# Kernel optimization log

Measured on AMD Instinct MI355X. Metric: run time of the kernel, lower is better.

## Reference

```python
import jax, jax.numpy as jnp
import numpy as np

N, D = 8192, 128

def setup_inputs() -> dict:
    key = jax.random.key(0)
    kq, kk, kv = jax.random.split(key, 3)
    return {
        "query": jax.random.normal(kq, (N, D), dtype=jnp.float32),
        "key": jax.random.normal(kk, (N, D), dtype=jnp.float32),
        "value": jax.random.normal(kv, (N, D), dtype=jnp.float32),
    }

def reference(query, key, value):
    # FlashAttentionV1 computes exact (non-causal, unmasked) softmax attention:
    # softmax(Q K^T / sqrt(d)) V, via tiled online softmax. The math is
    # identical to the dense formulation below.
    d = query.shape[-1]
    scores = jnp.einsum('qd,kd->qk', query, key) / jnp.sqrt(jnp.asarray(d, query.dtype))
    probs = jax.nn.softmax(scores, axis=-1)
    return jnp.einsum('qk,kd->qd', probs, value)
```

## Files before the change

### kernel.cpp

```cpp
#include <hip/hip_runtime.h>

#define NTOK 8192
#define DH   128
#define QBLK 128
#define KVB  64

typedef __attribute__((ext_vector_type(8)))  short bf16x8;
typedef __attribute__((ext_vector_type(16))) float f32x16;
typedef __attribute__((ext_vector_type(4)))  unsigned short u16x4;

typedef __attribute__((address_space(1))) const void gv_t;
typedef __attribute__((address_space(3))) void sv_t;

static __device__ __forceinline__ unsigned short f2bf(float x) {
  union { float f; unsigned int u; } a; a.f = x;
  unsigned int r = a.u + 0x7FFFu + ((a.u >> 16) & 1u);
  return (unsigned short)(r >> 16);
}

static __device__ __forceinline__ unsigned pk2(float lo, float hi) {
  unsigned r;
  asm("v_cvt_pk_bf16_f32 %0, %1, %2" : "=v"(r) : "v"(lo), "v"(hi));
  return r;
}

static __device__ __forceinline__ f32x16 zero16() {
  f32x16 v;
  #pragma unroll
  for (int i = 0; i < 16; ++i) v[i] = 0.f;
  return v;
}

__global__ __launch_bounds__(256)
void fa_prep(const float* __restrict__ Kg, const float* __restrict__ Vg,
             char* __restrict__ Kimg, char* __restrict__ Vimg)
{
  const int t = blockIdx.x;
  const int tid = threadIdx.x;

  {
    const int krow = tid >> 2;
    const int kcg  = (tid & 3) * 32;
    const float* src = Kg + ((size_t)t * KVB + krow) * DH + kcg;
    char* drow = Kimg + (size_t)t * 16384 + krow * 256;
    const int sw = (krow & 15) << 4;
    #pragma unroll
    for (int w = 0; w < 4; ++w) {
      float4 a = *reinterpret_cast<const float4*>(src + w * 8);
      float4 b = *reinterpret_cast<const float4*>(src + w * 8 + 4);
      union { bf16x8 v; unsigned short u[8]; } f;
      f.u[0] = f2bf(a.x); f.u[1] = f2bf(a.y); f.u[2] = f2bf(a.z); f.u[3] = f2bf(a.w);
      f.u[4] = f2bf(b.x); f.u[5] = f2bf(b.y); f.u[6] = f2bf(b.z); f.u[7] = f2bf(b.w);
      *reinterpret_cast<bf16x8*>(drow + ((kcg * 2 + w * 16) ^ sw)) = f.v;
    }
  }

  {
    #pragma unroll
    for (int it = 0; it < 2; ++it) {
      int task = tid + it * 256;
      int kvl  = (task & 15) * 4;
      int d0   = (task >> 4) * 4;
      const float* src = Vg + ((size_t)t * KVB + kvl) * DH + d0;
      float4 r0 = *reinterpret_cast<const float4*>(src);
      float4 r1 = *reinterpret_cast<const float4*>(src + DH);
      float4 r2 = *reinterpret_cast<const float4*>(src + 2 * DH);
      float4 r3 = *reinterpret_cast<const float4*>(src + 3 * DH);
      char* base = Vimg + (size_t)t * 16384;
      const int bb = kvl * 2;
      { int d = d0 + 0;
        u16x4 w4 = (u16x4){f2bf(r0.x), f2bf(r1.x), f2bf(r2.x), f2bf(r3.x)};
        *reinterpret_cast<u16x4*>(base + d * 128 + (bb ^ ((d & 15) << 3))) = w4; }
      { int d = d0 + 1;
        u16x4 w4 = (u16x4){f2bf(r0.y), f2bf(r1.y), f2bf(r2.y), f2bf(r3.y)};
        *reinterpret_cast<u16x4*>(base + d * 128 + (bb ^ ((d & 15) << 3))) = w4; }
      { int d = d0 + 2;
        u16x4 w4 = (u16x4){f2bf(r0.z), f2bf(r1.z), f2bf(r2.z), f2bf(r3.z)};
        *reinterpret_cast<u16x4*>(base + d * 128 + (bb ^ ((d & 15) << 3))) = w4; }
      { int d = d0 + 3;
        u16x4 w4 = (u16x4){f2bf(r0.w), f2bf(r1.w), f2bf(r2.w), f2bf(r3.w)};
        *reinterpret_cast<u16x4*>(base + d * 128 + (bb ^ ((d & 15) << 3))) = w4; }
    }
  }
}

static __device__ __forceinline__ void softmax_half(
    const f32x16& st, float& m_run, float& l_run, f32x16* oacc,
    bf16x8& pfa, bf16x8& pfb)
{
  float pmax = st[0];
  #pragma unroll
  for (int r = 1; r < 16; ++r) pmax = fmaxf(pmax, st[r]);
  pmax = fmaxf(pmax, __shfl_xor(pmax, 32));
  if (!__all(pmax <= m_run + 8.f)) {
    const float m_new = fmaxf(m_run, pmax);
    const float corr  = (m_run > -1e30f) ? exp2f(m_run - m_new) : 0.f;
    l_run *= corr;
    #pragma unroll
    for (int i = 0; i < 4; ++i) oacc[i] = oacc[i] * corr;
    m_run = m_new;
  }
  float psum = 0.f;
  unsigned w[8];
  #pragma unroll
  for (int i = 0; i < 8; ++i) {
    const float e0 = exp2f(st[2 * i]     - m_run);
    const float e1 = exp2f(st[2 * i + 1] - m_run);
    psum += e0 + e1;
    w[i] = pk2(e0, e1);
  }
  psum += __shfl_xor(psum, 32);
  l_run += psum;
  union { bf16x8 v; unsigned u[4]; } fa, fb;
  fa.u[0] = w[0]; fa.u[1] = w[1]; fa.u[2] = w[2]; fa.u[3] = w[3];
  fb.u[0] = w[4]; fb.u[1] = w[5]; fb.u[2] = w[6]; fb.u[3] = w[7];
  pfa = fa.v; pfb = fb.v;
}

__global__ __launch_bounds__(256, 2)
void fa_fwd(const float* __restrict__ Qg, const char* __restrict__ Kimg,
            const char* __restrict__ Vimg, float* __restrict__ Od,
            float* __restrict__ Mp, float* __restrict__ Lp,
            int ksplit, int chunk_len)
{
  __shared__ __align__(16) char smem[2][32768];
  const int tid  = threadIdx.x;
  const int lane = tid & 63;
  const int wv   = tid >> 6;
  const int l31  = lane & 31;
  const int hi   = lane >> 5;

  const int q     = blockIdx.x * QBLK + wv * 32 + l31;
  const int chunk = blockIdx.y;
  const float QSCALE = 0.1275313310087464f;

  const int tile0 = (chunk * chunk_len) >> 6;
  const int nst   = chunk_len >> 6;

  bf16x8 qf[8];
  {
    const float* qs = Qg + (size_t)q * DH + hi * 8;
    #pragma unroll
    for (int kc = 0; kc < 8; ++kc) {
      float4 a = *reinterpret_cast<const float4*>(qs + kc * 16);
      float4 b = *reinterpret_cast<const float4*>(qs + kc * 16 + 4);
      union { bf16x8 v; unsigned u[4]; } f;
      f.u[0] = pk2(a.x * QSCALE, a.y * QSCALE);
      f.u[1] = pk2(a.z * QSCALE, a.w * QSCALE);
      f.u[2] = pk2(b.x * QSCALE, b.y * QSCALE);
      f.u[3] = pk2(b.z * QSCALE, b.w * QSCALE);
      qf[kc] = f.v;
    }
  }

  const char* gbase = (wv < 2 ? Kimg : Vimg);
  const size_t goff = (size_t)(wv & 1) * 8192 + (size_t)lane * 16;
  const int    loff = (wv < 2 ? 0 : 16384) + (wv & 1) * 8192;

#define STAGE(B, T) do {                                                      \
    const char* _s = gbase + (size_t)(T) * 16384 + goff;                      \
    char* _d = &smem[B][loff];                                                \
    _Pragma("unroll")                                                         \
    for (int _i = 0; _i < 8; ++_i)                                            \
      __builtin_amdgcn_global_load_lds((gv_t*)(_s + _i * 1024),               \
                                       (sv_t*)(_d + _i * 1024), 16, 0, 0);    \
  } while (0)

  STAGE(0, tile0);
  if (nst > 1) STAGE(1, tile0 + 1);

  f32x16 oacc[4];
  #pragma unroll
  for (int i = 0; i < 4; ++i) oacc[i] = zero16();
  float m_run = -INFINITY, l_run = 0.f;

  int cur = 0;
  for (int t = 0; t < nst; ++t) {
    if (t + 1 < nst) asm volatile("s_waitcnt vmcnt(8)" ::: "memory");
    else             asm volatile("s_waitcnt vmcnt(0)" ::: "memory");
    __builtin_amdgcn_sched_barrier(0);
    __builtin_amdgcn_s_barrier();

    const char* smK = smem[cur];
    const char* smV = smem[cur] + 16384;
    const int swk = (l31 & 15) << 4;
    const int swv = (l31 & 15) << 3;

    f32x16 st0 = zero16(), st1 = zero16();
    __builtin_amdgcn_s_setprio(1);
    #pragma unroll
    for (int kc = 0; kc < 8; ++kc) {
      const int cb = (kc * 32 + hi * 16) ^ swk;
      bf16x8 a0 = *reinterpret_cast<const bf16x8*>(smK + l31 * 256 + cb);
      st0 = __builtin_amdgcn_mfma_f32_32x32x16_bf16(a0, qf[kc], st0, 0, 0, 0);
      bf16x8 a1 = *reinterpret_cast<const bf16x8*>(smK + (l31 + 32) * 256 + cb);
      st1 = __builtin_amdgcn_mfma_f32_32x32x16_bf16(a1, qf[kc], st1, 0, 0, 0);
    }
    __builtin_amdgcn_s_setprio(0);

    bf16x8 pf0a, pf0b;
    softmax_half(st0, m_run, l_run, oacc, pf0a, pf0b);
    __builtin_amdgcn_s_setprio(1);
    #pragma unroll
    for (int c = 0; c < 2; ++c) {
      const bf16x8 pb = c ? pf0b : pf0a;
      #pragma unroll
      for (int dt = 0; dt < 4; ++dt) {
        const char* vb = smV + (dt * 32 + l31) * 128;
        union { bf16x8 v; u16x4 h[2]; } a;
        a.h[0] = *reinterpret_cast<const u16x4*>(vb + ((c * 32 + 8 * hi) ^ swv));
        a.h[1] = *reinterpret_cast<const u16x4*>(vb + ((c * 32 + 16 + 8 * hi) ^ swv));
        oacc[dt] = __builtin_amdgcn_mfma_f32_32x32x16_bf16(a.v, pb, oacc[dt], 0, 0, 0);
      }
    }
    __builtin_amdgcn_s_setprio(0);

    bf16x8 pf1a, pf1b;
    softmax_half(st1, m_run, l_run, oacc, pf1a, pf1b);
    __builtin_amdgcn_s_setprio(1);
    #pragma unroll
    for (int c = 2; c < 4; ++c) {
      const bf16x8 pb = (c & 1) ? pf1b : pf1a;
      #pragma unroll
      for (int dt = 0; dt < 4; ++dt) {
        const char* vb = smV + (dt * 32 + l31) * 128;
        union { bf16x8 v; u16x4 h[2]; } a;
        a.h[0] = *reinterpret_cast<const u16x4*>(vb + ((c * 32 + 8 * hi) ^ swv));
        a.h[1] = *reinterpret_cast<const u16x4*>(vb + ((c * 32 + 16 + 8 * hi) ^ swv));
        oacc[dt] = __builtin_amdgcn_mfma_f32_32x32x16_bf16(a.v, pb, oacc[dt], 0, 0, 0);
      }
    }
    __builtin_amdgcn_s_setprio(0);

    __builtin_amdgcn_s_barrier();
    if (t + 2 < nst) STAGE(cur, tile0 + t + 2);
    cur ^= 1;
  }
#undef STAGE

  char* base = &smem[0][0] + wv * 16384;
  const float scale = (ksplit == 1) ? (1.f / l_run) : 1.f;
  #pragma unroll
  for (int dt = 0; dt < 4; ++dt)
    #pragma unroll
    for (int rg = 0; rg < 4; ++rg)
      #pragma unroll
      for (int j = 0; j < 4; ++j) {
        const int d = dt * 32 + rg * 8 + hi * 4 + j;
        *reinterpret_cast<float*>(base + d * 128 + l31 * 4) =
            oacc[dt][rg * 4 + j] * scale;
      }
  const int qloc = lane >> 1;
  const int dh   = lane & 1;
  float* dst = ((ksplit == 1) ? Od : Od + (size_t)chunk * NTOK * DH)
               + (size_t)(blockIdx.x * QBLK + wv * 32 + qloc) * DH + dh * 64;
  #pragma unroll
  for (int i4 = 0; i4 < 16; ++i4) {
    float4 v;
    v.x = *reinterpret_cast<float*>(base + (dh * 64 + i4 * 4 + 0) * 128 + qloc * 4);
    v.y = *reinterpret_cast<float*>(base + (dh * 64 + i4 * 4 + 1) * 128 + qloc * 4);
    v.z = *reinterpret_cast<float*>(base + (dh * 64 + i4 * 4 + 2) * 128 + qloc * 4);
    v.w = *reinterpret_cast<float*>(base + (dh * 64 + i4 * 4 + 3) * 128 + qloc * 4);
    *reinterpret_cast<float4*>(dst + i4 * 4) = v;
  }
  if (ksplit > 1 && lane < 32) {
    const int qg = blockIdx.x * QBLK + wv * 32 + lane;
    Mp[chunk * NTOK + qg] = m_run;
    Lp[chunk * NTOK + qg] = l_run;
  }
}

__global__ __launch_bounds__(256)
void fa_combine(const float* __restrict__ Op, const float* __restrict__ Mp,
                const float* __restrict__ Lp, float* __restrict__ out, int ksplit)
{
  const int gid = blockIdx.x * 256 + threadIdx.x;
  const int q   = gid >> 5;
  const int dv  = (gid & 31) * 4;
  float mx = -INFINITY;
  for (int c = 0; c < ksplit; ++c) mx = fmaxf(mx, Mp[c * NTOK + q]);
  float den = 0.f;
  float ax = 0.f, ay = 0.f, az = 0.f, aw = 0.f;
  for (int c = 0; c < ksplit; ++c) {
    const float w = exp2f(Mp[c * NTOK + q] - mx);
    den += w * Lp[c * NTOK + q];
    float4 o = *reinterpret_cast<const float4*>(Op + (size_t)c * NTOK * DH + (size_t)q * DH + dv);
    ax += w * o.x; ay += w * o.y; az += w * o.z; aw += w * o.w;
  }
  const float r = 1.f / den;
  float4 res; res.x = ax * r; res.y = ay * r; res.z = az * r; res.w = aw * r;
  *reinterpret_cast<float4*>(out + (size_t)q * DH + dv) = res;
}

extern "C" void kernel_launch(void* const* d_in, const int* in_sizes, int n_in,
                              void* d_out, int out_size, void* d_ws, size_t ws_size,
                              hipStream_t stream)
{
  const float* Q = (const float*)d_in[0];
  const float* K = (const float*)d_in[1];
  const float* V = (const float*)d_in[2];
  float* out = (float*)d_out;

  auto need = [](size_t ks) {
    return ks * (size_t)NTOK * DH * 4 + 2 * ks * (size_t)NTOK * 4;
  };
  int KS = (ws_size >= need(8)) ? 8 : (ws_size >= need(4)) ? 4 : 2;

  char* Kimg = (char*)d_out;
  char* Vimg = Kimg + (size_t)NTOK * 256;

  float* Op = (float*)d_ws;
  float* Mp = Op + (size_t)KS * NTOK * DH;
  float* Lp = Mp + (size_t)KS * NTOK;

  fa_prep<<<NTOK / KVB, 256, 0, stream>>>(K, V, Kimg, Vimg);
  fa_fwd<<<dim3(NTOK / QBLK, KS), 256, 0, stream>>>(Q, Kimg, Vimg, Op, Mp, Lp,
                                                    KS, NTOK / KS);
  fa_combine<<<NTOK * DH / 4 / 256, 256, 0, stream>>>(Op, Mp, Lp, out, KS);
}
```

Measured before the change: 75.33 us.

## Double query block to 8 waves sharing KV tiles and raise K-split

Doubles the query block to 256 rows and the workgroup to 512 threads, so eight waves share each staged K/V tile and each wave issues half as many global-to-LDS loads. Removes the per-tile cross-half shuffles for the row sum, deferring that reduction to the epilogue; the max shuffle now runs only when a rescale is needed. The epilogue runs in two barrier-separated phases to reuse the LDS buffer, and the default KV split rises to 16. The tighter launch bounds (512 threads, 4 blocks) may force heavy register spilling given the accumulators held per wave.

```diff
diff --git a/kernel.cpp b/kernel.cpp
--- a/kernel.cpp
+++ b/kernel.cpp
@@ -2,7 +2,7 @@
 
 #define NTOK 8192
 #define DH   128
-#define QBLK 128
+#define QBLK 256
 #define KVB  64
 
 typedef __attribute__((ext_vector_type(8)))  short bf16x8;
@@ -91,8 +91,8 @@
   float pmax = st[0];
   #pragma unroll
   for (int r = 1; r < 16; ++r) pmax = fmaxf(pmax, st[r]);
-  pmax = fmaxf(pmax, __shfl_xor(pmax, 32));
   if (!__all(pmax <= m_run + 8.f)) {
+    pmax = fmaxf(pmax, __shfl_xor(pmax, 32));
     const float m_new = fmaxf(m_run, pmax);
     const float corr  = (m_run > -1e30f) ? exp2f(m_run - m_new) : 0.f;
     l_run *= corr;
@@ -109,7 +109,6 @@
     psum += e0 + e1;
     w[i] = pk2(e0, e1);
   }
-  psum += __shfl_xor(psum, 32);
   l_run += psum;
   union { bf16x8 v; unsigned u[4]; } fa, fb;
   fa.u[0] = w[0]; fa.u[1] = w[1]; fa.u[2] = w[2]; fa.u[3] = w[3];
@@ -117,7 +116,7 @@
   pfa = fa.v; pfb = fb.v;
 }
 
-__global__ __launch_bounds__(256, 2)
+__global__ __launch_bounds__(512, 4)
 void fa_fwd(const float* __restrict__ Qg, const char* __restrict__ Kimg,
             const char* __restrict__ Vimg, float* __restrict__ Od,
             float* __restrict__ Mp, float* __restrict__ Lp,
@@ -153,15 +152,15 @@
     }
   }
 
-  const char* gbase = (wv < 2 ? Kimg : Vimg);
-  const size_t goff = (size_t)(wv & 1) * 8192 + (size_t)lane * 16;
-  const int    loff = (wv < 2 ? 0 : 16384) + (wv & 1) * 8192;
+  const char* gbase = (wv < 4 ? Kimg : Vimg);
+  const size_t goff = (size_t)(wv & 3) * 4096 + (size_t)lane * 16;
+  const int    loff = (wv < 4 ? 0 : 16384) + (wv & 3) * 4096;
 
 #define STAGE(B, T) do {                                                      \
     const char* _s = gbase + (size_t)(T) * 16384 + goff;                      \
     char* _d = &smem[B][loff];                                                \
     _Pragma("unroll")                                                         \
-    for (int _i = 0; _i < 8; ++_i)                                            \
+    for (int _i = 0; _i < 4; ++_i)                                            \
       __builtin_amdgcn_global_load_lds((gv_t*)(_s + _i * 1024),               \
                                        (sv_t*)(_d + _i * 1024), 16, 0, 0);    \
   } while (0)
@@ -176,7 +175,7 @@
 
   int cur = 0;
   for (int t = 0; t < nst; ++t) {
-    if (t + 1 < nst) asm volatile("s_waitcnt vmcnt(8)" ::: "memory");
+    if (t + 1 < nst) asm volatile("s_waitcnt vmcnt(4)" ::: "memory");
     else             asm volatile("s_waitcnt vmcnt(0)" ::: "memory");
     __builtin_amdgcn_sched_barrier(0);
     __builtin_amdgcn_s_barrier();
@@ -238,35 +237,47 @@
   }
 #undef STAGE
 
-  char* base = &smem[0][0] + wv * 16384;
-  const float scale = (ksplit == 1) ? (1.f / l_run) : 1.f;
-  #pragma unroll
-  for (int dt = 0; dt < 4; ++dt)
-    #pragma unroll
-    for (int rg = 0; rg < 4; ++rg)
-      #pragma unroll
-      for (int j = 0; j < 4; ++j) {
-        const int d = dt * 32 + rg * 8 + hi * 4 + j;
-        *reinterpret_cast<float*>(base + d * 128 + l31 * 4) =
-            oacc[dt][rg * 4 + j] * scale;
-      }
-  const int qloc = lane >> 1;
-  const int dh   = lane & 1;
-  float* dst = ((ksplit == 1) ? Od : Od + (size_t)chunk * NTOK * DH)
-               + (size_t)(blockIdx.x * QBLK + wv * 32 + qloc) * DH + dh * 64;
-  #pragma unroll
-  for (int i4 = 0; i4 < 16; ++i4) {
-    float4 v;
-    v.x = *reinterpret_cast<float*>(base + (dh * 64 + i4 * 4 + 0) * 128 + qloc * 4);
-    v.y = *reinterpret_cast<float*>(base + (dh * 64 + i4 * 4 + 1) * 128 + qloc * 4);
-    v.z = *reinterpret_cast<float*>(base + (dh * 64 + i4 * 4 + 2) * 128 + qloc * 4);
-    v.w = *reinterpret_cast<float*>(base + (dh * 64 + i4 * 4 + 3) * 128 + qloc * 4);
-    *reinterpret_cast<float4*>(dst + i4 * 4) = v;
-  }
+  const float l_tot = l_run + __shfl_xor(l_run, 32);
+
+  char* base = &smem[0][0] + (wv & 3) * 16384;
+  const float scale = (ksplit == 1) ? (1.f / l_tot) : 1.f;
+  float* dstb = ((ksplit == 1) ? Od : Od + (size_t)chunk * NTOK * DH);
+
+#define EPILOGUE() do {                                                        \
+    _Pragma("unroll")                                                          \
+    for (int dt = 0; dt < 4; ++dt)                                             \
+      _Pragma("unroll")                                                        \
+      for (int rg = 0; rg < 4; ++rg)                                           \
+        _Pragma("unroll")                                                      \
+        for (int j = 0; j < 4; ++j) {                                          \
+          const int d = dt * 32 + rg * 8 + hi * 4 + j;                         \
+          *reinterpret_cast<float*>(base + d * 128 + l31 * 4) =                \
+              oacc[dt][rg * 4 + j] * scale;                                    \
+        }                                                                      \
+    const int qloc = lane >> 1;                                                \
+    const int dh   = lane & 1;                                                 \
+    float* dst = dstb + (size_t)(blockIdx.x * QBLK + wv * 32 + qloc) * DH      \
+                 + dh * 64;                                                    \
+    _Pragma("unroll")                                                          \
+    for (int i4 = 0; i4 < 16; ++i4) {                                          \
+      float4 v;                                                                \
+      v.x = *reinterpret_cast<float*>(base + (dh*64 + i4*4 + 0)*128 + qloc*4); \
+      v.y = *reinterpret_cast<float*>(base + (dh*64 + i4*4 + 1)*128 + qloc*4); \
+      v.z = *reinterpret_cast<float*>(base + (dh*64 + i4*4 + 2)*128 + qloc*4); \
+      v.w = *reinterpret_cast<float*>(base + (dh*64 + i4*4 + 3)*128 + qloc*4); \
+      *reinterpret_cast<float4*>(dst + i4 * 4) = v;                            \
+    }                                                                          \
+  } while (0)
+
+  if (wv < 4) EPILOGUE();
+  __builtin_amdgcn_s_barrier();
+  if (wv >= 4) EPILOGUE();
+#undef EPILOGUE
+
   if (ksplit > 1 && lane < 32) {
     const int qg = blockIdx.x * QBLK + wv * 32 + lane;
     Mp[chunk * NTOK + qg] = m_run;
-    Lp[chunk * NTOK + qg] = l_run;
+    Lp[chunk * NTOK + qg] = l_tot;
   }
 }
 
@@ -304,7 +315,7 @@
   auto need = [](size_t ks) {
     return ks * (size_t)NTOK * DH * 4 + 2 * ks * (size_t)NTOK * 4;
   };
-  int KS = (ws_size >= need(8)) ? 8 : (ws_size >= need(4)) ? 4 : 2;
+  int KS = (ws_size >= need(16)) ? 16 : (ws_size >= need(8)) ? 8 : 4;
 
   char* Kimg = (char*)d_out;
   char* Vimg = Kimg + (size_t)NTOK * 256;
@@ -314,7 +325,7 @@
   float* Lp = Mp + (size_t)KS * NTOK;
 
   fa_prep<<<NTOK / KVB, 256, 0, stream>>>(K, V, Kimg, Vimg);
-  fa_fwd<<<dim3(NTOK / QBLK, KS), 256, 0, stream>>>(Q, Kimg, Vimg, Op, Mp, Lp,
+  fa_fwd<<<dim3(NTOK / QBLK, KS), 512, 0, stream>>>(Q, Kimg, Vimg, Op, Mp, Lp,
                                                     KS, NTOK / KS);
   fa_combine<<<NTOK * DH / 4 / 256, 256, 0, stream>>>(Op, Mp, Lp, out, KS);
 }
```

After: 117.3 us. +55.7%, slower.

## Halve KV tile to 32, raise occupancy, remap grid for split-K locality

Applied to the files above, without the earlier changes.

Shrinks the KV tile from 64 to 32 keys and rebuilds the K/V image layout and swizzle to match. This halves LDS per block so the launch bound can request 4 blocks per CU. The per-tile softmax drops the cross-half shuffles, keeps per-half row sums and combines them once at the end. It also raises the split-K factor to 16 when workspace allows, flattens the grid with a chunk-interleaved block mapping, and splits the output transpose into two barrier phases to fit the smaller LDS. The cost is more loop iterations with less work each, more partial outputs for the combine kernel to read, and higher register pressure under the stricter launch bound.

```diff
diff --git a/kernel.cpp b/kernel.cpp
--- a/kernel.cpp
+++ b/kernel.cpp
@@ -3,7 +3,7 @@
 #define NTOK 8192
 #define DH   128
 #define QBLK 128
-#define KVB  64
+#define KVB  32
 
 typedef __attribute__((ext_vector_type(8)))  short bf16x8;
 typedef __attribute__((ext_vector_type(16))) float f32x16;
@@ -39,13 +39,13 @@
   const int tid = threadIdx.x;
 
   {
-    const int krow = tid >> 2;
-    const int kcg  = (tid & 3) * 32;
+    const int krow = tid >> 3;
+    const int kcg  = (tid & 7) * 16;
     const float* src = Kg + ((size_t)t * KVB + krow) * DH + kcg;
-    char* drow = Kimg + (size_t)t * 16384 + krow * 256;
+    char* drow = Kimg + (size_t)t * 8192 + krow * 256;
     const int sw = (krow & 15) << 4;
     #pragma unroll
-    for (int w = 0; w < 4; ++w) {
+    for (int w = 0; w < 2; ++w) {
       float4 a = *reinterpret_cast<const float4*>(src + w * 8);
       float4 b = *reinterpret_cast<const float4*>(src + w * 8 + 4);
       union { bf16x8 v; unsigned short u[8]; } f;
@@ -56,43 +56,39 @@
   }
 
   {
-    #pragma unroll
-    for (int it = 0; it < 2; ++it) {
-      int task = tid + it * 256;
-      int kvl  = (task & 15) * 4;
-      int d0   = (task >> 4) * 4;
-      const float* src = Vg + ((size_t)t * KVB + kvl) * DH + d0;
-      float4 r0 = *reinterpret_cast<const float4*>(src);
-      float4 r1 = *reinterpret_cast<const float4*>(src + DH);
-      float4 r2 = *reinterpret_cast<const float4*>(src + 2 * DH);
-      float4 r3 = *reinterpret_cast<const float4*>(src + 3 * DH);
-      char* base = Vimg + (size_t)t * 16384;
-      const int bb = kvl * 2;
-      { int d = d0 + 0;
-        u16x4 w4 = (u16x4){f2bf(r0.x), f2bf(r1.x), f2bf(r2.x), f2bf(r3.x)};
-        *reinterpret_cast<u16x4*>(base + d * 128 + (bb ^ ((d & 15) << 3))) = w4; }
-      { int d = d0 + 1;
-        u16x4 w4 = (u16x4){f2bf(r0.y), f2bf(r1.y), f2bf(r2.y), f2bf(r3.y)};
-        *reinterpret_cast<u16x4*>(base + d * 128 + (bb ^ ((d & 15) << 3))) = w4; }
-      { int d = d0 + 2;
-        u16x4 w4 = (u16x4){f2bf(r0.z), f2bf(r1.z), f2bf(r2.z), f2bf(r3.z)};
-        *reinterpret_cast<u16x4*>(base + d * 128 + (bb ^ ((d & 15) << 3))) = w4; }
-      { int d = d0 + 3;
-        u16x4 w4 = (u16x4){f2bf(r0.w), f2bf(r1.w), f2bf(r2.w), f2bf(r3.w)};
-        *reinterpret_cast<u16x4*>(base + d * 128 + (bb ^ ((d & 15) << 3))) = w4; }
-    }
-  }
-}
-
-static __device__ __forceinline__ void softmax_half(
+    const int kvl = (tid & 7) * 4;
+    const int d0  = (tid >> 3) * 4;
+    const float* src = Vg + ((size_t)t * KVB + kvl) * DH + d0;
+    float4 r0 = *reinterpret_cast<const float4*>(src);
+    float4 r1 = *reinterpret_cast<const float4*>(src + DH);
+    float4 r2 = *reinterpret_cast<const float4*>(src + 2 * DH);
+    float4 r3 = *reinterpret_cast<const float4*>(src + 3 * DH);
+    char* base = Vimg + (size_t)t * 8192;
+    const int bb = kvl * 2;
+    { int d = d0 + 0;
+      u16x4 w4 = (u16x4){f2bf(r0.x), f2bf(r1.x), f2bf(r2.x), f2bf(r3.x)};
+      *reinterpret_cast<u16x4*>(base + d * 64 + (bb ^ (((d >> 1) & 7) << 3))) = w4; }
+    { int d = d0 + 1;
+      u16x4 w4 = (u16x4){f2bf(r0.y), f2bf(r1.y), f2bf(r2.y), f2bf(r3.y)};
+      *reinterpret_cast<u16x4*>(base + d * 64 + (bb ^ (((d >> 1) & 7) << 3))) = w4; }
+    { int d = d0 + 2;
+      u16x4 w4 = (u16x4){f2bf(r0.z), f2bf(r1.z), f2bf(r2.z), f2bf(r3.z)};
+      *reinterpret_cast<u16x4*>(base + d * 64 + (bb ^ (((d >> 1) & 7) << 3))) = w4; }
+    { int d = d0 + 3;
+      u16x4 w4 = (u16x4){f2bf(r0.w), f2bf(r1.w), f2bf(r2.w), f2bf(r3.w)};
+      *reinterpret_cast<u16x4*>(base + d * 64 + (bb ^ (((d >> 1) & 7) << 3))) = w4; }
+  }
+}
+
+static __device__ __forceinline__ void softmax_tile(
     const f32x16& st, float& m_run, float& l_run, f32x16* oacc,
     bf16x8& pfa, bf16x8& pfb)
 {
   float pmax = st[0];
   #pragma unroll
   for (int r = 1; r < 16; ++r) pmax = fmaxf(pmax, st[r]);
-  pmax = fmaxf(pmax, __shfl_xor(pmax, 32));
   if (!__all(pmax <= m_run + 8.f)) {
+    pmax = fmaxf(pmax, __shfl_xor(pmax, 32));
     const float m_new = fmaxf(m_run, pmax);
     const float corr  = (m_run > -1e30f) ? exp2f(m_run - m_new) : 0.f;
     l_run *= corr;
@@ -109,7 +105,6 @@
     psum += e0 + e1;
     w[i] = pk2(e0, e1);
   }
-  psum += __shfl_xor(psum, 32);
   l_run += psum;
   union { bf16x8 v; unsigned u[4]; } fa, fb;
   fa.u[0] = w[0]; fa.u[1] = w[1]; fa.u[2] = w[2]; fa.u[3] = w[3];
@@ -117,25 +112,30 @@
   pfa = fa.v; pfb = fb.v;
 }
 
-__global__ __launch_bounds__(256, 2)
+__global__ __launch_bounds__(256, 4)
 void fa_fwd(const float* __restrict__ Qg, const char* __restrict__ Kimg,
             const char* __restrict__ Vimg, float* __restrict__ Od,
             float* __restrict__ Mp, float* __restrict__ Lp,
             int ksplit, int chunk_len)
 {
-  __shared__ __align__(16) char smem[2][32768];
+  __shared__ __align__(16) char smem[2][16384];
   const int tid  = threadIdx.x;
   const int lane = tid & 63;
   const int wv   = tid >> 6;
   const int l31  = lane & 31;
   const int hi   = lane >> 5;
 
-  const int q     = blockIdx.x * QBLK + wv * 32 + l31;
-  const int chunk = blockIdx.y;
+  const int cpx   = ksplit >> 3;
+  const int id    = blockIdx.x;
+  const int chunk = (id & 7) * cpx + ((id >> 3) & (cpx - 1));
+  const int bx    = id >> (3 + (cpx >> 1));
+
+  const int q0blk = bx * QBLK;
+  const int q     = q0blk + wv * 32 + l31;
   const float QSCALE = 0.1275313310087464f;
 
-  const int tile0 = (chunk * chunk_len) >> 6;
-  const int nst   = chunk_len >> 6;
+  const int tile0 = (chunk * chunk_len) >> 5;
+  const int nst   = chunk_len >> 5;
 
   bf16x8 qf[8];
   {
@@ -154,14 +154,14 @@
   }
 
   const char* gbase = (wv < 2 ? Kimg : Vimg);
-  const size_t goff = (size_t)(wv & 1) * 8192 + (size_t)lane * 16;
-  const int    loff = (wv < 2 ? 0 : 16384) + (wv & 1) * 8192;
+  const size_t goff = (size_t)(wv & 1) * 4096 + (size_t)lane * 16;
+  const int    loff = (wv < 2 ? 0 : 8192) + (wv & 1) * 4096;
 
 #define STAGE(B, T) do {                                                      \
-    const char* _s = gbase + (size_t)(T) * 16384 + goff;                      \
+    const char* _s = gbase + (size_t)(T) * 8192 + goff;                       \
     char* _d = &smem[B][loff];                                                \
     _Pragma("unroll")                                                         \
-    for (int _i = 0; _i < 8; ++_i)                                            \
+    for (int _i = 0; _i < 4; ++_i)                                            \
       __builtin_amdgcn_global_load_lds((gv_t*)(_s + _i * 1024),               \
                                        (sv_t*)(_d + _i * 1024), 16, 0, 0);    \
   } while (0)
@@ -176,57 +176,39 @@
 
   int cur = 0;
   for (int t = 0; t < nst; ++t) {
-    if (t + 1 < nst) asm volatile("s_waitcnt vmcnt(8)" ::: "memory");
+    if (t + 1 < nst) asm volatile("s_waitcnt vmcnt(4)" ::: "memory");
     else             asm volatile("s_waitcnt vmcnt(0)" ::: "memory");
     __builtin_amdgcn_sched_barrier(0);
     __builtin_amdgcn_s_barrier();
 
     const char* smK = smem[cur];
-    const char* smV = smem[cur] + 16384;
+    const char* smV = smem[cur] + 8192;
     const int swk = (l31 & 15) << 4;
-    const int swv = (l31 & 15) << 3;
-
-    f32x16 st0 = zero16(), st1 = zero16();
+
+    f32x16 st0 = zero16();
     __builtin_amdgcn_s_setprio(1);
     #pragma unroll
     for (int kc = 0; kc < 8; ++kc) {
-      const int cb = (kc * 32 + hi * 16) ^ swk;
-      bf16x8 a0 = *reinterpret_cast<const bf16x8*>(smK + l31 * 256 + cb);
+      bf16x8 a0 = *reinterpret_cast<const bf16x8*>(
+          smK + l31 * 256 + ((kc * 32 + hi * 16) ^ swk));
       st0 = __builtin_amdgcn_mfma_f32_32x32x16_bf16(a0, qf[kc], st0, 0, 0, 0);
-      bf16x8 a1 = *reinterpret_cast<const bf16x8*>(smK + (l31 + 32) * 256 + cb);
-      st1 = __builtin_amdgcn_mfma_f32_32x32x16_bf16(a1, qf[kc], st1, 0, 0, 0);
     }
     __builtin_amdgcn_s_setprio(0);
 
-    bf16x8 pf0a, pf0b;
-    softmax_half(st0, m_run, l_run, oacc, pf0a, pf0b);
+    bf16x8 pfa, pfb;
+    softmax_tile(st0, m_run, l_run, oacc, pfa, pfb);
     __builtin_amdgcn_s_setprio(1);
     #pragma unroll
     for (int c = 0; c < 2; ++c) {
-      const bf16x8 pb = c ? pf0b : pf0a;
+      const bf16x8 pb = c ? pfb : pfa;
       #pragma unroll
       for (int dt = 0; dt < 4; ++dt) {
-        const char* vb = smV + (dt * 32 + l31) * 128;
+        const int d  = dt * 32 + l31;
+        const char* vb = smV + d * 64;
+        const int sw = ((d >> 1) & 7) << 3;
         union { bf16x8 v; u16x4 h[2]; } a;
-        a.h[0] = *reinterpret_cast<const u16x4*>(vb + ((c * 32 + 8 * hi) ^ swv));
-        a.h[1] = *reinterpret_cast<const u16x4*>(vb + ((c * 32 + 16 + 8 * hi) ^ swv));
-        oacc[dt] = __builtin_amdgcn_mfma_f32_32x32x16_bf16(a.v, pb, oacc[dt], 0, 0, 0);
-      }
-    }
-    __builtin_amdgcn_s_setprio(0);
-
-    bf16x8 pf1a, pf1b;
-    softmax_half(st1, m_run, l_run, oacc, pf1a, pf1b);
-    __builtin_amdgcn_s_setprio(1);
-    #pragma unroll
-    for (int c = 2; c < 4; ++c) {
-      const bf16x8 pb = (c & 1) ? pf1b : pf1a;
-      #pragma unroll
-      for (int dt = 0; dt < 4; ++dt) {
-        const char* vb = smV + (dt * 32 + l31) * 128;
-        union { bf16x8 v; u16x4 h[2]; } a;
-        a.h[0] = *reinterpret_cast<const u16x4*>(vb + ((c * 32 + 8 * hi) ^ swv));
-        a.h[1] = *reinterpret_cast<const u16x4*>(vb + ((c * 32 + 16 + 8 * hi) ^ swv));
+        a.h[0] = *reinterpret_cast<const u16x4*>(vb + ((c * 32 + 8 * hi) ^ sw));
+        a.h[1] = *reinterpret_cast<const u16x4*>(vb + ((c * 32 + 16 + 8 * hi) ^ sw));
         oacc[dt] = __builtin_amdgcn_mfma_f32_32x32x16_bf16(a.v, pb, oacc[dt], 0, 0, 0);
       }
     }
@@ -238,35 +220,51 @@
   }
 #undef STAGE
 
-  char* base = &smem[0][0] + wv * 16384;
-  const float scale = (ksplit == 1) ? (1.f / l_run) : 1.f;
-  #pragma unroll
-  for (int dt = 0; dt < 4; ++dt)
-    #pragma unroll
-    for (int rg = 0; rg < 4; ++rg)
+  const float l_tot = l_run + __shfl_xor(l_run, 32);
+  const float scale = (ksplit == 1) ? (1.f / l_tot) : 1.f;
+  float* dstB = (ksplit == 1) ? Od : Od + (size_t)chunk * NTOK * DH;
+
+  char* base = &smem[0][0] + (wv & 1) * 16384;
+  const int qloc4 = lane >> 2;
+  const int s4    = lane & 3;
+  #pragma unroll
+  for (int ph = 0; ph < 2; ++ph) {
+    __builtin_amdgcn_s_barrier();
+    if ((wv >> 1) == ph) {
       #pragma unroll
-      for (int j = 0; j < 4; ++j) {
-        const int d = dt * 32 + rg * 8 + hi * 4 + j;
-        *reinterpret_cast<float*>(base + d * 128 + l31 * 4) =
-            oacc[dt][rg * 4 + j] * scale;
+      for (int dt = 0; dt < 4; ++dt)
+        #pragma unroll
+        for (int rg = 0; rg < 4; ++rg)
+          #pragma unroll
+          for (int j = 0; j < 4; ++j) {
+            const int d = dt * 32 + rg * 8 + hi * 4 + j;
+            *reinterpret_cast<float*>(base + d * 128 + l31 * 4) =
+                oacc[dt][rg * 4 + j] * scale;
+          }
+      asm volatile("s_waitcnt lgkmcnt(0)" ::: "memory");
+      __builtin_amdgcn_sched_barrier(0);
+      #pragma unroll
+      for (int qh = 0; qh < 2; ++qh) {
+        const int qloc = qh * 16 + qloc4;
+        float* dst = dstB + (size_t)(q0blk + wv * 32 + qloc) * DH;
+        #pragma unroll
+        for (int i = 0; i < 8; ++i) {
+          const int dd = s4 * 4 + i * 16;
+          float4 v;
+          v.x = *reinterpret_cast<float*>(base + (dd + 0) * 128 + qloc * 4);
+          v.y = *reinterpret_cast<float*>(base + (dd + 1) * 128 + qloc * 4);
+          v.z = *reinterpret_cast<float*>(base + (dd + 2) * 128 + qloc * 4);
+          v.w = *reinterpret_cast<float*>(base + (dd + 3) * 128 + qloc * 4);
+          *reinterpret_cast<float4*>(dst + dd) = v;
+        }
       }
-  const int qloc = lane >> 1;
-  const int dh   = lane & 1;
-  float* dst = ((ksplit == 1) ? Od : Od + (size_t)chunk * NTOK * DH)
-               + (size_t)(blockIdx.x * QBLK + wv * 32 + qloc) * DH + dh * 64;
-  #pragma unroll
-  for (int i4 = 0; i4 < 16; ++i4) {
-    float4 v;
-    v.x = *reinterpret_cast<float*>(base + (dh * 64 + i4 * 4 + 0) * 128 + qloc * 4);
-    v.y = *reinterpret_cast<float*>(base + (dh * 64 + i4 * 4 + 1) * 128 + qloc * 4);
-    v.z = *reinterpret_cast<float*>(base + (dh * 64 + i4 * 4 + 2) * 128 + qloc * 4);
-    v.w = *reinterpret_cast<float*>(base + (dh * 64 + i4 * 4 + 3) * 128 + qloc * 4);
-    *reinterpret_cast<float4*>(dst + i4 * 4) = v;
-  }
+    }
+  }
+
   if (ksplit > 1 && lane < 32) {
-    const int qg = blockIdx.x * QBLK + wv * 32 + lane;
+    const int qg = q0blk + wv * 32 + lane;
     Mp[chunk * NTOK + qg] = m_run;
-    Lp[chunk * NTOK + qg] = l_run;
+    Lp[chunk * NTOK + qg] = l_tot;
   }
 }
 
@@ -304,7 +302,7 @@
   auto need = [](size_t ks) {
     return ks * (size_t)NTOK * DH * 4 + 2 * ks * (size_t)NTOK * 4;
   };
-  int KS = (ws_size >= need(8)) ? 8 : (ws_size >= need(4)) ? 4 : 2;
+  int KS = (ws_size >= need(16)) ? 16 : 8;
 
   char* Kimg = (char*)d_out;
   char* Vimg = Kimg + (size_t)NTOK * 256;
@@ -314,7 +312,7 @@
   float* Lp = Mp + (size_t)KS * NTOK;
 
   fa_prep<<<NTOK / KVB, 256, 0, stream>>>(K, V, Kimg, Vimg);
-  fa_fwd<<<dim3(NTOK / QBLK, KS), 256, 0, stream>>>(Q, Kimg, Vimg, Op, Mp, Lp,
-                                                    KS, NTOK / KS);
+  fa_fwd<<<(NTOK / QBLK) * KS, 256, 0, stream>>>(Q, Kimg, Vimg, Op, Mp, Lp,
+                                                 KS, NTOK / KS);
   fa_combine<<<NTOK * DH / 4 / 256, 256, 0, stream>>>(Op, Mp, Lp, out, KS);
 }
```

Result: slower. 113.2 us (+50.3%).
